# Kernel optimization log

Measured on AMD Instinct MI355X. Metric: run time of the kernel, lower is better.

## Reference

```python
import jax, jax.numpy as jnp
import numpy as np

N_FEAT = 128      # node_feat_size
HID = 128         # hidden_size
NUM_SEM = 64
N_ITER = 2
E_TYPES = 8
MAX_CHILDS = 65536
NUM_EDGES = 1048576


def setup_inputs() -> dict:
    key = jax.random.key(0)
    ks = jax.random.split(key, 12)
    d_in = N_FEAT + NUM_SEM
    inp = {
        "child_feats": jax.random.normal(ks[0], (1, MAX_CHILDS, d_in), jnp.float32),
        "child_exists": jax.random.uniform(ks[1], (1, MAX_CHILDS, 1), jnp.float32),
        "edge_type_onehot": jax.random.uniform(ks[2], (1, NUM_EDGES, E_TYPES), jnp.float32),
        "edge_indices": jax.random.randint(ks[3], (1, NUM_EDGES, 2), 0, MAX_CHILDS, jnp.int32),
        # learned params (PyTorch Linear: y = x @ W.T + b; store transposed)
        "W_child": jax.random.normal(ks[4], (d_in, HID), jnp.float32) / np.sqrt(d_in),
        "b_child": jnp.zeros((HID,), jnp.float32),
        "W_edge": jax.random.normal(ks[5], (N_ITER, 2 * HID + E_TYPES, HID), jnp.float32) / np.sqrt(2 * HID + E_TYPES),
        "b_edge": jnp.zeros((N_ITER, HID), jnp.float32),
        "W_parent": jax.random.normal(ks[6], ((N_ITER + 1) * HID, N_FEAT), jnp.float32) / np.sqrt((N_ITER + 1) * HID),
        "b_parent": jnp.zeros((N_FEAT,), jnp.float32),
    }
    return inp


def reference(child_feats, child_exists, edge_type_onehot, edge_indices,
              W_child, b_child, W_edge, b_edge, W_parent, b_parent):
    # batch_size == 1 enforced by original module
    x = jax.nn.relu(child_feats[0] @ W_child + b_child) * child_exists[0]  # (N, H)
    src = edge_indices[0, :, 0]  # (E,)
    dst = edge_indices[0, :, 1]  # (E,)
    ef = edge_type_onehot[0]     # (E, T)

    # node_symmetric_type == 'max' readout
    parent_feats = [jnp.max(x, axis=0)]
    for i in range(N_ITER):
        # gather endpoints, concat with edge features, small MLP
        nef = jnp.concatenate([x[src], x[dst], ef], axis=1)          # (E, 2H+T)
        nef = jax.nn.relu(nef @ W_edge[i] + b_edge[i])               # (E, H)
        # edge_symmetric_type == 'sum' -> scatter_add to source nodes
        x = jax.ops.segment_sum(nef, src, num_segments=MAX_CHILDS)   # (N, H)
        parent_feats.append(jnp.max(x, axis=0))

    parent_feat = jnp.concatenate(parent_feats)[None, :]             # (1, (I+1)*H)
    return jax.nn.relu(parent_feat @ W_parent + b_parent)            # (1, node_feat)
```

## Files before the change

### kernel.cpp

```cpp
#include <hip/hip_runtime.h>
#include <hip/hip_bf16.h>

#define HID 128
#define DIN 192
#define NCH 65536
#define NE  1048576

typedef __bf16 bfrag __attribute__((ext_vector_type(8)));
typedef float  ffrag __attribute__((ext_vector_type(4)));

static __device__ __forceinline__ __bf16 f2bf(float x) { return (__bf16)x; }
static __device__ __forceinline__ unsigned pk2(float a, float b) {
    __bf16 b0 = f2bf(a), b1 = f2bf(b);
    return (unsigned)*(unsigned short*)&b0 | ((unsigned)*(unsigned short*)&b1 << 16);
}
static __device__ __forceinline__ unsigned char f2q(float x) {
    return (unsigned char)(__builtin_amdgcn_cvt_pk_fp8_f32(x, x, 0, false) & 0xff);
}

struct FragsQ { long d[4]; long ef; };

__global__ __launch_bounds__(256) void k_childhist(
    const float* __restrict__ cf, const float* __restrict__ exists,
    const float* __restrict__ Wc, const float* __restrict__ bc,
    __bf16* __restrict__ xA, unsigned int* __restrict__ pmax,
    const int* __restrict__ eidx, int* __restrict__ deg)
{
    if (blockIdx.x >= 1024) {
        const int base = (blockIdx.x - 1024) * 1024 + threadIdx.x;
        #pragma unroll
        for (int k = 0; k < 4; ++k)
            atomicAdd(&deg[eidx[2 * (base + k * 256)]], 1);
        return;
    }

    __shared__ __bf16 Wl[6 * 8 * 64 * 8];
    __shared__ float  bl[HID];
    __shared__ unsigned int cm[HID];
    const int t = threadIdx.x;

    for (int idx = t; idx < DIN * HID; idx += 256) {
        int k = idx >> 7, h = idx & 127;
        int kt = k >> 5, kk = k & 31;
        int lane = ((kk >> 3) << 4) | (h & 15);
        Wl[((((kt * 8) + (h >> 4)) * 64 + lane) << 3) | (kk & 7)] = f2bf(Wc[idx]);
    }
    for (int idx = t; idx < HID; idx += 256) { bl[idx] = bc[idx]; cm[idx] = 0u; }
    __syncthreads();

    const int wave = t >> 6, lane = t & 63;
    const int m = lane & 15, quad = lane >> 4;

    const int tile = blockIdx.x * 4 + wave;
    const int r0 = tile << 4;
    const int row = r0 + m;

    ffrag acc[8];
    #pragma unroll
    for (int u = 0; u < 8; ++u)
        #pragma unroll
        for (int r = 0; r < 4; ++r) acc[u][r] = 0.f;

    const float* arow = cf + (size_t)row * DIN + quad * 8;
    #pragma unroll
    for (int kt = 0; kt < 6; ++kt) {
        float4 f0 = *(const float4*)(arow + kt * 32);
        float4 f1 = *(const float4*)(arow + kt * 32 + 4);
        bfrag a;
        a[0]=f2bf(f0.x); a[1]=f2bf(f0.y); a[2]=f2bf(f0.z); a[3]=f2bf(f0.w);
        a[4]=f2bf(f1.x); a[5]=f2bf(f1.y); a[6]=f2bf(f1.z); a[7]=f2bf(f1.w);
        #pragma unroll
        for (int u = 0; u < 8; ++u) {
            bfrag b = *(const bfrag*)(&Wl[(((kt * 8 + u) * 64 + lane) << 3)]);
            acc[u] = __builtin_amdgcn_mfma_f32_16x16x32_bf16(a, b, acc[u], 0, 0, 0);
        }
    }

    float mxu[8];
    #pragma unroll
    for (int u = 0; u < 8; ++u) mxu[u] = 0.f;

    #pragma unroll
    for (int r = 0; r < 4; ++r) {
        int er = r0 + quad * 4 + r;
        float exv = exists[er];
        __bf16* orow = xA + (size_t)er * HID;
        #pragma unroll
        for (int u = 0; u < 8; ++u) {
            int col = u * 16 + m;
            float v = fmaxf(acc[u][r] + bl[col], 0.f) * exv;
            orow[col] = f2bf(v);
            mxu[u] = fmaxf(mxu[u], v);
        }
    }
    #pragma unroll
    for (int u = 0; u < 8; ++u) {
        float v = mxu[u];
        v = fmaxf(v, __shfl_xor(v, 16));
        v = fmaxf(v, __shfl_xor(v, 32));
        if (quad == 0) atomicMax(&cm[u * 16 + m], __float_as_uint(v));
    }
    __syncthreads();
    if (t < HID) atomicMax(&pmax[t], cm[t]);
}

__global__ __launch_bounds__(256) void k_scan1(
    const int* __restrict__ deg, int* __restrict__ bsum)
{
    const int b = blockIdx.x, t = threadIdx.x;
    int v = deg[b * 256 + t];
    #pragma unroll
    for (int o = 1; o < 64; o <<= 1) v += __shfl_xor(v, o);
    __shared__ int ws[4];
    if ((t & 63) == 0) ws[t >> 6] = v;
    __syncthreads();
    if (t == 0) bsum[b] = ws[0] + ws[1] + ws[2] + ws[3];
}

__global__ __launch_bounds__(256) void k_scan2(
    const int* __restrict__ bsum, int* __restrict__ bbase)
{
    __shared__ int sc[256];
    const int t = threadIdx.x;
    int v = bsum[t];
    sc[t] = v;
    __syncthreads();
    for (int o = 1; o < 256; o <<= 1) {
        int u = (t >= o) ? sc[t - o] : 0;
        __syncthreads();
        sc[t] += u;
        __syncthreads();
    }
    bbase[t] = sc[t] - v;
}

__global__ __launch_bounds__(256) void k_scan3(
    const int* __restrict__ deg, const int* __restrict__ bbase,
    int* __restrict__ off, int* __restrict__ cursor)
{
    __shared__ int sc[256];
    const int b = blockIdx.x, t = threadIdx.x;
    int v = deg[b * 256 + t];
    sc[t] = v;
    __syncthreads();
    for (int o = 1; o < 256; o <<= 1) {
        int u = (t >= o) ? sc[t - o] : 0;
        __syncthreads();
        sc[t] += u;
        __syncthreads();
    }
    int excl = bbase[b] + sc[t] - v;
    off[b * 256 + t] = excl;
    cursor[b * 256 + t] = excl;
    if (b == 255 && t == 255) off[NCH] = excl + v;
}

__global__ __launch_bounds__(256) void k_scatter(
    const int* __restrict__ eidx, int* __restrict__ cursor,
    const float* __restrict__ ef,
    int* __restrict__ dsts, unsigned char* __restrict__ efs8)
{
    int e = blockIdx.x * 256 + threadIdx.x;
    int s = eidx[2 * e], d = eidx[2 * e + 1];
    const float4* p = (const float4*)(ef + (size_t)e * 8);
    float4 f0 = p[0], f1 = p[1];
    int pos = atomicAdd(&cursor[s], 1);
    dsts[pos] = d;
    unsigned p01 = __builtin_amdgcn_cvt_pk_fp8_f32(f0.x, f0.y, 0, false) & 0xffff;
    unsigned p23 = __builtin_amdgcn_cvt_pk_fp8_f32(f0.z, f0.w, 0, false) & 0xffff;
    unsigned p45 = __builtin_amdgcn_cvt_pk_fp8_f32(f1.x, f1.y, 0, false) & 0xffff;
    unsigned p67 = __builtin_amdgcn_cvt_pk_fp8_f32(f1.z, f1.w, 0, false) & 0xffff;
    unsigned long long v = (unsigned long long)(p01 | (p23 << 16))
                         | ((unsigned long long)(p45 | (p67 << 16)) << 32);
    *(unsigned long long*)(efs8 + (size_t)pos * 8) = v;
}

__global__ __launch_bounds__(256) void k_src(
    const __bf16* __restrict__ xCur, const float* __restrict__ We,
    const float* __restrict__ be, __bf16* __restrict__ St2,
    unsigned char* __restrict__ Dq)
{
    __shared__ __bf16 Wl[4 * 8 * 64 * 8];
    __shared__ float  bl[HID];
    const int t = threadIdx.x;
    const int wave = t >> 6, lane = t & 63;
    const int m = lane & 15, quad = lane >> 4;
    const int tile = blockIdx.x * 4 + wave;
    const int r0 = tile << 4;
    const int row = r0 + m;

    for (int idx = t; idx < 128 * HID; idx += 256) {
        int k = idx >> 7, h = idx & 127;
        int kt = k >> 5, kk = k & 31;
        int ln = ((kk >> 3) << 4) | (h & 15);
        Wl[((((kt * 8) + (h >> 4)) * 64 + ln) << 3) | (kk & 7)] = f2bf(We[idx]);
    }
    for (int idx = t; idx < HID; idx += 256) bl[idx] = be[idx];
    __syncthreads();

    bfrag a[4];
    const __bf16* ar = xCur + (size_t)row * HID + quad * 8;
    #pragma unroll
    for (int kt = 0; kt < 4; ++kt) a[kt] = *(const bfrag*)(ar + kt * 32);

    ffrag acc[8];
    #pragma unroll
    for (int u = 0; u < 8; ++u)
        #pragma unroll
        for (int r = 0; r < 4; ++r) acc[u][r] = 0.f;

    #pragma unroll
    for (int kt = 0; kt < 4; ++kt)
        #pragma unroll
        for (int u = 0; u < 8; ++u) {
            bfrag b = *(const bfrag*)(&Wl[(((kt * 8 + u) * 64 + lane) << 3)]);
            acc[u] = __builtin_amdgcn_mfma_f32_16x16x32_bf16(a[kt], b, acc[u], 0, 0, 0);
        }
    #pragma unroll
    for (int r = 0; r < 4; ++r) {
        int node = r0 + quad * 4 + r;
        bfrag pk;
        #pragma unroll
        for (int u = 0; u < 8; ++u) pk[u] = f2bf(acc[u][r] + bl[u * 16 + m]);
        *(bfrag*)(St2 + ((size_t)node * 16 + m) * 8) = pk;
    }
    __syncthreads();

    for (int idx = t; idx < 128 * HID; idx += 256) {
        int k = idx >> 7, h = idx & 127;
        int kt = k >> 5, kk = k & 31;
        int ln = ((kk >> 3) << 4) | (h & 15);
        Wl[((((kt * 8) + (h >> 4)) * 64 + ln) << 3) | (kk & 7)] = f2bf(We[(size_t)(128 + k) * HID + h]);
    }
    __syncthreads();

    #pragma unroll
    for (int u = 0; u < 8; ++u)
        #pragma unroll
        for (int r = 0; r < 4; ++r) acc[u][r] = 0.f;

    #pragma unroll
    for (int kt = 0; kt < 4; ++kt)
        #pragma unroll
        for (int u = 0; u < 8; ++u) {
            bfrag b = *(const bfrag*)(&Wl[(((kt * 8 + u) * 64 + lane) << 3)]);
            acc[u] = __builtin_amdgcn_mfma_f32_16x16x32_bf16(a[kt], b, acc[u], 0, 0, 0);
        }
    #pragma unroll
    for (int r = 0; r < 4; ++r) {
        int node = r0 + quad * 4 + r;
        unsigned char* orow = Dq + (size_t)node * 128;
        #pragma unroll
        for (int u = 0; u < 8; ++u) orow[u * 16 + m] = f2q(acc[u][r]);
    }
}

__global__ __launch_bounds__(256) void k_edge2(
    const unsigned char* __restrict__ Dq,
    const int*    __restrict__ offs,
    const int*    __restrict__ dsts,
    const unsigned char* __restrict__ efs8,
    const __bf16* __restrict__ St2,
    const float*  __restrict__ We,
    __bf16* __restrict__ xNext,
    unsigned int* __restrict__ pmax, int stage)
{
    __shared__ unsigned char Wf[8 * 16 * 8];
    __shared__ unsigned int cm[HID];
    const int t = threadIdx.x;

    if (t < HID) cm[t] = 0u;
    for (int idx = t; idx < 8 * HID; idx += 256) {
        int k2 = idx >> 7, h = idx & 127;
        Wf[((((h >> 4) * 16) + (h & 15)) << 3) + k2] = f2q(We[(size_t)(256 + k2) * HID + h]);
    }
    __syncthreads();

    const int wave = t >> 6, lane = t & 63;
    const int m = lane & 15, quad = lane >> 4;
    const int gw = blockIdx.x * 4 + wave;
    const int n0 = gw * 4;

    const long BevQ = (quad == (m >> 3))     ? ((long)0x38 << (8 * (m & 7))) : 0L;
    const long BodQ = (quad == 2 + (m >> 3)) ? ((long)0x38 << (8 * (m & 7))) : 0L;

    const int o0 = offs[n0],     o1 = offs[n0 + 1], o2 = offs[n0 + 2];
    const int o3 = offs[n0 + 3], o4 = offs[n0 + 4];

    auto selo = [&](int q) -> int {
        return (q <= 0) ? o0 : (q == 1) ? o1 : (q == 2) ? o2 : (q == 3) ? o3 : o4;
    };

    float mxu[8];
    #pragma unroll
    for (int u = 0; u < 8; ++u) mxu[u] = 0.f;

    if (o0 < o4) {
        const int dvA = dsts[min(o0 + lane, o4 - 1)];
        const int dvB = dsts[min(o0 + 64 + lane, o4 - 1)];

        auto LOADT = [&](int j) -> FragsQ {
            FragsQ f;
            int jl = j + m; jl = (jl < o4) ? jl : (o4 - 1);
            int rel = jl - o0;
            int dA = __shfl(dvA, rel & 63);
            int dB = __shfl(dvB, rel & 63);
            int dm;
            if (rel < 64)       dm = dA;
            else if (rel < 128) dm = dB;
            else                dm = dsts[jl];
            const unsigned char* rd = Dq + (size_t)dm * 128 + quad * 8;
            f.d[0] = *(const long*)(rd);
            f.d[1] = *(const long*)(rd + 32);
            f.d[2] = *(const long*)(rd + 64);
            f.d[3] = *(const long*)(rd + 96);
            f.ef = (quad == 0) ? *(const long*)(efs8 + (size_t)jl * 8) : 0L;
            return f;
        };

        int ci = 0;
        while (selo(ci) == selo(ci + 1)) ++ci;
        int cj = selo(ci);

        bfrag sb = *(const bfrag*)(St2 + ((size_t)(n0 + ci) * 16 + m) * 8);
        float part[8];
        #pragma unroll
        for (int u = 0; u < 8; ++u) part[u] = 0.f;

        FragsQ aC = LOADT(cj);

        for (;;) {
            const int cEnd = selo(ci + 1);
            int ni = ci, nj = cj + 16;
            if (nj >= cEnd) {
                ni = ci + 1;
                while (ni < 4 && selo(ni) == selo(ni + 1)) ++ni;
                nj = (ni < 4) ? selo(ni) : 0;
            }
            const bool hn = (ni < 4);
            FragsQ aN;
            if (hn) aN = LOADT(nj);

            ffrag acc[8];
            #pragma unroll
            for (int u = 0; u < 8; ++u) {
                float s = (float)sb[u];
                acc[u][0] = s; acc[u][1] = s; acc[u][2] = s; acc[u][3] = s;
            }
            #pragma unroll
            for (int u = 0; u < 8; ++u)
                acc[u] = __builtin_amdgcn_mfma_f32_16x16x32_fp8_fp8(
                    aC.d[u >> 1], (u & 1) ? BodQ : BevQ, acc[u], 0, 0, 0);
            #pragma unroll
            for (int u = 0; u < 8; ++u) {
                long b = *(const long*)(&Wf[((u << 4) + m) << 3]);
                acc[u] = __builtin_amdgcn_mfma_f32_16x16x32_fp8_fp8(aC.ef, b, acc[u], 0, 0, 0);
            }

            const int rb = cj + quad * 4;
            #pragma unroll
            for (int r = 0; r < 4; ++r) {
                if (rb + r < cEnd) {
                    #pragma unroll
                    for (int u = 0; u < 8; ++u)
                        part[u] += fmaxf(acc[u][r], 0.f);
                }
            }

            if (!hn || ni != ci) {
                float tot[8];
                #pragma unroll
                for (int u = 0; u < 8; ++u) {
                    float v = part[u];
                    v += __shfl_xor(v, 16);
                    v += __shfl_xor(v, 32);
                    tot[u] = v;
                    mxu[u] = fmaxf(mxu[u], v);
                }
                float sA = (quad == 0) ? tot[0] : (quad == 1) ? tot[2] : (quad == 2) ? tot[4] : tot[6];
                float sB = (quad == 0) ? tot[1] : (quad == 1) ? tot[3] : (quad == 2) ? tot[5] : tot[7];
                const int n = n0 + ci, u0 = quad * 2;
                xNext[(size_t)n * HID + u0 * 16 + m]      = f2bf(sA);
                xNext[(size_t)n * HID + u0 * 16 + 16 + m] = f2bf(sB);
                if (hn) {
                    sb = *(const bfrag*)(St2 + ((size_t)(n0 + ni) * 16 + m) * 8);
                    #pragma unroll
                    for (int u = 0; u < 8; ++u) part[u] = 0.f;
                }
            }
            if (!hn) break;
            aC = aN; ci = ni; cj = nj;
        }
    }

    {
        const int u0 = quad * 2;
        const __bf16 zz = (__bf16)0.f;
        if (o0 == o1) { xNext[(size_t)(n0+0)*HID + u0*16 + m] = zz; xNext[(size_t)(n0+0)*HID + u0*16 + 16 + m] = zz; }
        if (o1 == o2) { xNext[(size_t)(n0+1)*HID + u0*16 + m] = zz; xNext[(size_t)(n0+1)*HID + u0*16 + 16 + m] = zz; }
        if (o2 == o3) { xNext[(size_t)(n0+2)*HID + u0*16 + m] = zz; xNext[(size_t)(n0+2)*HID + u0*16 + 16 + m] = zz; }
        if (o3 == o4) { xNext[(size_t)(n0+3)*HID + u0*16 + m] = zz; xNext[(size_t)(n0+3)*HID + u0*16 + 16 + m] = zz; }
    }

    #pragma unroll
    for (int u = 0; u < 8; ++u) {
        float v = mxu[u];
        v = fmaxf(v, __shfl_xor(v, 16));
        v = fmaxf(v, __shfl_xor(v, 32));
        if (quad == 0) atomicMax(&cm[u * 16 + m], __float_as_uint(v));
    }
    __syncthreads();
    if (t < HID) atomicMax(&pmax[stage * HID + t], cm[t]);
}

__global__ __launch_bounds__(256) void k_edge_at(
    const __bf16* __restrict__ xA, const int* __restrict__ eidx,
    const float* __restrict__ ef, const float* __restrict__ We,
    const float* __restrict__ be, float* __restrict__ xNew)
{
    __shared__ __bf16 Wl[9 * 8 * 64 * 8];
    __shared__ float  bl[HID];
    const int t = threadIdx.x;
    for (int idx = t; idx < 8 * 64 * 8; idx += 256) Wl[8 * 8 * 64 * 8 + idx] = (__bf16)0.f;
    __syncthreads();
    for (int idx = t; idx < 256 * HID; idx += 256) {
        int k = idx >> 7, h = idx & 127;
        int kt = k >> 5, kk = k & 31;
        int lane = ((kk >> 3) << 4) | (h & 15);
        Wl[((((kt * 8) + (h >> 4)) * 64 + lane) << 3) | (kk & 7)] = f2bf(We[idx]);
    }
    for (int idx = t; idx < 8 * HID; idx += 256) {
        int k2 = idx >> 7, h = idx & 127;
        Wl[((((8 * 8) + (h >> 4)) * 64 + (h & 15)) << 3) | k2] = f2bf(We[(256 + k2) * HID + h]);
    }
    for (int idx = t; idx < HID; idx += 256) bl[idx] = be[idx];
    __syncthreads();

    const int wave = t >> 6, lane = t & 63;
    const int m = lane & 15, quad = lane >> 4;
    for (int c = 0; c < 8; ++c) {
        const int e0 = blockIdx.x * 512 + c * 64 + wave * 16;
        const int e  = e0 + m;
        const int src = eidx[2 * e], dst = eidx[2 * e + 1];
        const __bf16* rs = xA + (size_t)src * HID;
        const __bf16* rd = xA + (size_t)dst * HID;
        bfrag a[9];
        #pragma unroll
        for (int kt = 0; kt < 4; ++kt) a[kt] = *(const bfrag*)(rs + kt * 32 + quad * 8);
        #pragma unroll
        for (int kt = 4; kt < 8; ++kt) a[kt] = *(const bfrag*)(rd + (kt - 4) * 32 + quad * 8);
        {
            bfrag z;
            #pragma unroll
            for (int q = 0; q < 8; ++q) z[q] = (__bf16)0.f;
            if (quad == 0) {
                const float4* p = (const float4*)(ef + (size_t)e * 8);
                float4 f0 = p[0], f1 = p[1];
                z[0]=f2bf(f0.x); z[1]=f2bf(f0.y); z[2]=f2bf(f0.z); z[3]=f2bf(f0.w);
                z[4]=f2bf(f1.x); z[5]=f2bf(f1.y); z[6]=f2bf(f1.z); z[7]=f2bf(f1.w);
            }
            a[8] = z;
        }
        ffrag acc[8];
        #pragma unroll
        for (int u = 0; u < 8; ++u)
            #pragma unroll
            for (int r = 0; r < 4; ++r) acc[u][r] = 0.f;
        #pragma unroll
        for (int kt = 0; kt < 9; ++kt)
            #pragma unroll
            for (int u = 0; u < 8; ++u) {
                bfrag b = *(const bfrag*)(&Wl[(((kt * 8 + u) * 64 + lane) << 3)]);
                acc[u] = __builtin_amdgcn_mfma_f32_16x16x32_bf16(a[kt], b, acc[u], 0, 0, 0);
            }
        #pragma unroll
        for (int r = 0; r < 4; ++r) {
            int er = e0 + quad * 4 + r;
            int sr = eidx[2 * er];
            float* outrow = xNew + (size_t)sr * HID;
            #pragma unroll
            for (int u = 0; u < 8; ++u) {
                int col = u * 16 + m;
                atomicAdd(outrow + col, fmaxf(acc[u][r] + bl[col], 0.f));
            }
        }
    }
}

__global__ __launch_bounds__(256) void k_fin(
    float* __restrict__ xNew, __bf16* __restrict__ xA,
    unsigned int* __restrict__ pmax, int stage, int flags)
{
    const int t = threadIdx.x;
    const size_t total  = (size_t)NCH * HID;
    const size_t stride = (size_t)gridDim.x * 256;
    float mx = 0.f;
    for (size_t i = (size_t)blockIdx.x * 256 + t; i < total; i += stride) {
        float v = xNew[i];
        mx = fmaxf(mx, v);
        if (flags & 1) xA[i] = f2bf(v);
        if (flags & 2) xNew[i] = 0.f;
    }
    __shared__ float red[256];
    red[t] = mx;
    __syncthreads();
    if (t < 128) {
        float v = fmaxf(red[t], red[t + 128]);
        atomicMax(&pmax[stage * HID + t], __float_as_uint(v));
    }
}

__global__ __launch_bounds__(128) void k_parent(
    const unsigned int* __restrict__ pmaxU,
    const float* __restrict__ Wp, const float* __restrict__ bp,
    float* __restrict__ out)
{
    __shared__ float pl[384];
    const int t = threadIdx.x;
    for (int i = t; i < 384; i += 128) pl[i] = __uint_as_float(pmaxU[i]);
    __syncthreads();
    float acc = bp[t];
    for (int j = 0; j < 384; ++j) acc += pl[j] * Wp[j * HID + t];
    out[t] = fmaxf(acc, 0.f);
}

extern "C" void kernel_launch(void* const* d_in, const int* in_sizes, int n_in,
                              void* d_out, int out_size, void* d_ws, size_t ws_size,
                              hipStream_t stream)
{
    const float* cf   = (const float*)d_in[0];
    const float* ex   = (const float*)d_in[1];
    const float* ef   = (const float*)d_in[2];
    const int*   eidx = (const int*)d_in[3];
    const float* Wc   = (const float*)d_in[4];
    const float* bc   = (const float*)d_in[5];
    const float* We   = (const float*)d_in[6];
    const float* be   = (const float*)d_in[7];
    const float* Wp   = (const float*)d_in[8];
    const float* bp   = (const float*)d_in[9];
    float* out = (float*)d_out;

    char* ws = (char*)d_ws;

    const size_t OFF_XA   = 0;
    const size_t OFF_XB   = OFF_XA   + (size_t)NCH * HID * 2;
    const size_t OFF_ST   = OFF_XB   + (size_t)NCH * HID * 2;
    const size_t OFF_EFS  = OFF_ST   + (size_t)NCH * HID * 2;
    const size_t OFF_DQ   = OFF_EFS  + (size_t)NE * 8;
    const size_t OFF_DST  = OFF_DQ   + (size_t)NCH * 128;
    const size_t OFF_OFFS = OFF_DST  + (size_t)NE * 4;
    const size_t OFF_DEG  = OFF_OFFS + 262400;
    const size_t OFF_CUR  = OFF_DEG  + 262144;
    const size_t OFF_PMAX = OFF_CUR  + 262144;
    const size_t OFF_BS   = OFF_PMAX + 2048;
    const size_t OFF_BB   = OFF_BS   + 1024;
    const size_t NEED     = OFF_BB   + 1024;

    if (ws_size >= NEED) {
        __bf16*        xA   = (__bf16*)(ws + OFF_XA);
        __bf16*        xB   = (__bf16*)(ws + OFF_XB);
        __bf16*        St2  = (__bf16*)(ws + OFF_ST);
        unsigned char* efs8 = (unsigned char*)(ws + OFF_EFS);
        unsigned char* Dq   = (unsigned char*)(ws + OFF_DQ);
        int*           dsts = (int*)   (ws + OFF_DST);
        int*           offs = (int*)   (ws + OFF_OFFS);
        int*           deg  = (int*)   (ws + OFF_DEG);
        int*           cur  = (int*)   (ws + OFF_CUR);
        unsigned int*  pmax = (unsigned int*)(ws + OFF_PMAX);
        int*           bsum = (int*)   (ws + OFF_BS);
        int*           bbas = (int*)   (ws + OFF_BB);

        hipMemsetAsync(pmax, 0, 384 * sizeof(unsigned int), stream);
        hipMemsetAsync(deg, 0, NCH * sizeof(int), stream);

        k_childhist<<<2048, 256, 0, stream>>>(cf, ex, Wc, bc, xA, pmax, eidx, deg);
        k_scan1  <<<256,  256, 0, stream>>>(deg, bsum);
        k_scan2  <<<1,    256, 0, stream>>>(bsum, bbas);
        k_scan3  <<<256,  256, 0, stream>>>(deg, bbas, offs, cur);
        k_scatter<<<4096, 256, 0, stream>>>(eidx, cur, ef, dsts, efs8);

        k_src    <<<1024, 256, 0, stream>>>(xA, We, be, St2, Dq);
        k_edge2  <<<4096, 256, 0, stream>>>(Dq, offs, dsts, efs8, St2, We, xB, pmax, 1);
        k_src    <<<1024, 256, 0, stream>>>(xB, We + 264 * HID, be + HID, St2, Dq);
        k_edge2  <<<4096, 256, 0, stream>>>(Dq, offs, dsts, efs8, St2, We + 264 * HID, xA, pmax, 2);
        k_parent <<<1,    128, 0, stream>>>(pmax, Wp, bp, out);
    } else {
        float*        xNew = (float*)ws;
        __bf16*       xA   = (__bf16*)(ws + (size_t)NCH * HID * 4);
        unsigned int* pmax = (unsigned int*)(ws + (size_t)NCH * HID * 6);

        hipMemsetAsync(pmax, 0, 384 * sizeof(unsigned int), stream);
        hipMemsetAsync(xNew, 0, (size_t)NCH * HID * 4, stream);

        k_childhist<<<1024, 256, 0, stream>>>(cf, ex, Wc, bc, xA, pmax, eidx, (int*)nullptr);
        k_edge_at<<<2048, 256, 0, stream>>>(xA, eidx, ef, We,             be,       xNew);
        k_fin    <<<512,  256, 0, stream>>>(xNew, xA, pmax, 1, 3);
        k_edge_at<<<2048, 256, 0, stream>>>(xA, eidx, ef, We + 264 * HID, be + HID, xNew);
        k_fin    <<<512,  256, 0, stream>>>(xNew, xA, pmax, 2, 0);
        k_parent <<<1,    128, 0, stream>>>(pmax, Wp, bp, out);
    }
}
```

Before: 538.6 us.

## Fuse scan and scatter kernels, restage weights, repack Dq for wider loads

Merges the scan2 and scan3 passes into one kernel in which every block redundantly scans the block sums. The edge scatter is folded into the first source-projection launch as extra blocks. The two memsets become one by placing pmax next to deg. Weight staging now writes whole 8-element bf16 fragments per thread, and the Dq fp8 layout is permuted so each lane reads two 16-byte vectors instead of four 8-byte loads. The aim is fewer launches, less launch and serialization overhead, and wider memory accesses, at the cost of redundant scan work in each block.

```diff
diff --git a/kernel.cpp b/kernel.cpp
--- a/kernel.cpp
+++ b/kernel.cpp
@@ -8,6 +8,7 @@
 
 typedef __bf16 bfrag __attribute__((ext_vector_type(8)));
 typedef float  ffrag __attribute__((ext_vector_type(4)));
+typedef long   lfrag2 __attribute__((ext_vector_type(2)));
 
 static __device__ __forceinline__ __bf16 f2bf(float x) { return (__bf16)x; }
 static __device__ __forceinline__ unsigned pk2(float a, float b) {
@@ -19,6 +20,20 @@
 }
 
 struct FragsQ { long d[4]; long ef; };
+
+static __device__ __forceinline__ void stage_wfrag(
+    __bf16* Wl, const float* W, int rowoff, int chunks, int t)
+{
+    for (int c = t; c < chunks; c += 256) {
+        int lane = c & 63, u = (c >> 6) & 7, kt = c >> 9;
+        int k0 = kt * 32 + ((lane >> 4) << 3), h = u * 16 + (lane & 15);
+        const float* src = W + (size_t)(rowoff + k0) * 128 + h;
+        bfrag f;
+        #pragma unroll
+        for (int j = 0; j < 8; ++j) f[j] = f2bf(src[(size_t)j * 128]);
+        *(bfrag*)(&Wl[(size_t)c << 3]) = f;
+    }
+}
 
 __global__ __launch_bounds__(256) void k_childhist(
     const float* __restrict__ cf, const float* __restrict__ exists,
@@ -39,12 +54,7 @@
     __shared__ unsigned int cm[HID];
     const int t = threadIdx.x;
 
-    for (int idx = t; idx < DIN * HID; idx += 256) {
-        int k = idx >> 7, h = idx & 127;
-        int kt = k >> 5, kk = k & 31;
-        int lane = ((kk >> 3) << 4) | (h & 15);
-        Wl[((((kt * 8) + (h >> 4)) * 64 + lane) << 3) | (kk & 7)] = f2bf(Wc[idx]);
-    }
+    stage_wfrag(Wl, Wc, 0, 3072, t);
     for (int idx = t; idx < HID; idx += 256) { bl[idx] = bc[idx]; cm[idx] = 0u; }
     __syncthreads();
 
@@ -117,84 +127,66 @@
     if (t == 0) bsum[b] = ws[0] + ws[1] + ws[2] + ws[3];
 }
 
-__global__ __launch_bounds__(256) void k_scan2(
-    const int* __restrict__ bsum, int* __restrict__ bbase)
-{
-    __shared__ int sc[256];
-    const int t = threadIdx.x;
-    int v = bsum[t];
-    sc[t] = v;
+__global__ __launch_bounds__(256) void k_scan23(
+    const int* __restrict__ deg, const int* __restrict__ bsum,
+    int* __restrict__ off, int* __restrict__ cursor)
+{
+    __shared__ int sb[256], sc[256];
+    const int b = blockIdx.x, t = threadIdx.x;
+    int w = bsum[t];
+    int v = deg[b * 256 + t];
+    sb[t] = w; sc[t] = v;
     __syncthreads();
     for (int o = 1; o < 256; o <<= 1) {
-        int u = (t >= o) ? sc[t - o] : 0;
+        int u1 = (t >= o) ? sb[t - o] : 0;
+        int u2 = (t >= o) ? sc[t - o] : 0;
         __syncthreads();
-        sc[t] += u;
+        sb[t] += u1; sc[t] += u2;
         __syncthreads();
     }
-    bbase[t] = sc[t] - v;
-}
-
-__global__ __launch_bounds__(256) void k_scan3(
-    const int* __restrict__ deg, const int* __restrict__ bbase,
-    int* __restrict__ off, int* __restrict__ cursor)
-{
-    __shared__ int sc[256];
-    const int b = blockIdx.x, t = threadIdx.x;
-    int v = deg[b * 256 + t];
-    sc[t] = v;
-    __syncthreads();
-    for (int o = 1; o < 256; o <<= 1) {
-        int u = (t >= o) ? sc[t - o] : 0;
-        __syncthreads();
-        sc[t] += u;
-        __syncthreads();
-    }
-    int excl = bbase[b] + sc[t] - v;
+    int bbase = (b == 0) ? 0 : sb[b - 1];
+    int excl = bbase + sc[t] - v;
     off[b * 256 + t] = excl;
     cursor[b * 256 + t] = excl;
     if (b == 255 && t == 255) off[NCH] = excl + v;
 }
 
-__global__ __launch_bounds__(256) void k_scatter(
+__global__ __launch_bounds__(256) void k_scsrc(
+    const __bf16* __restrict__ xCur, const float* __restrict__ We,
+    const float* __restrict__ be, __bf16* __restrict__ St2,
+    unsigned char* __restrict__ Dq,
     const int* __restrict__ eidx, int* __restrict__ cursor,
     const float* __restrict__ ef,
     int* __restrict__ dsts, unsigned char* __restrict__ efs8)
 {
-    int e = blockIdx.x * 256 + threadIdx.x;
-    int s = eidx[2 * e], d = eidx[2 * e + 1];
-    const float4* p = (const float4*)(ef + (size_t)e * 8);
-    float4 f0 = p[0], f1 = p[1];
-    int pos = atomicAdd(&cursor[s], 1);
-    dsts[pos] = d;
-    unsigned p01 = __builtin_amdgcn_cvt_pk_fp8_f32(f0.x, f0.y, 0, false) & 0xffff;
-    unsigned p23 = __builtin_amdgcn_cvt_pk_fp8_f32(f0.z, f0.w, 0, false) & 0xffff;
-    unsigned p45 = __builtin_amdgcn_cvt_pk_fp8_f32(f1.x, f1.y, 0, false) & 0xffff;
-    unsigned p67 = __builtin_amdgcn_cvt_pk_fp8_f32(f1.z, f1.w, 0, false) & 0xffff;
-    unsigned long long v = (unsigned long long)(p01 | (p23 << 16))
-                         | ((unsigned long long)(p45 | (p67 << 16)) << 32);
-    *(unsigned long long*)(efs8 + (size_t)pos * 8) = v;
-}
-
-__global__ __launch_bounds__(256) void k_src(
-    const __bf16* __restrict__ xCur, const float* __restrict__ We,
-    const float* __restrict__ be, __bf16* __restrict__ St2,
-    unsigned char* __restrict__ Dq)
-{
     __shared__ __bf16 Wl[4 * 8 * 64 * 8];
     __shared__ float  bl[HID];
     const int t = threadIdx.x;
+
+    if (blockIdx.x >= 1024) {
+        int e = (blockIdx.x - 1024) * 256 + t;
+        int s = eidx[2 * e], d = eidx[2 * e + 1];
+        const float4* p = (const float4*)(ef + (size_t)e * 8);
+        float4 f0 = p[0], f1 = p[1];
+        int pos = atomicAdd(&cursor[s], 1);
+        dsts[pos] = d;
+        unsigned p01 = __builtin_amdgcn_cvt_pk_fp8_f32(f0.x, f0.y, 0, false) & 0xffff;
+        unsigned p23 = __builtin_amdgcn_cvt_pk_fp8_f32(f0.z, f0.w, 0, false) & 0xffff;
+        unsigned p45 = __builtin_amdgcn_cvt_pk_fp8_f32(f1.x, f1.y, 0, false) & 0xffff;
+        unsigned p67 = __builtin_amdgcn_cvt_pk_fp8_f32(f1.z, f1.w, 0, false) & 0xffff;
+        unsigned long long v = (unsigned long long)(p01 | (p23 << 16))
+                             | ((unsigned long long)(p45 | (p67 << 16)) << 32);
+        *(unsigned long long*)(efs8 + (size_t)pos * 8) = v;
+        return;
+    }
+
     const int wave = t >> 6, lane = t & 63;
     const int m = lane & 15, quad = lane >> 4;
     const int tile = blockIdx.x * 4 + wave;
     const int r0 = tile << 4;
     const int row = r0 + m;
 
-    for (int idx = t; idx < 128 * HID; idx += 256) {
-        int k = idx >> 7, h = idx & 127;
-        int kt = k >> 5, kk = k & 31;
-        int ln = ((kk >> 3) << 4) | (h & 15);
-        Wl[((((kt * 8) + (h >> 4)) * 64 + ln) << 3) | (kk & 7)] = f2bf(We[idx]);
-    }
+    stage_wfrag(Wl, We, 0, 2048, t);
     for (int idx = t; idx < HID; idx += 256) bl[idx] = be[idx];
     __syncthreads();
 
@@ -226,12 +218,7 @@
     }
     __syncthreads();
 
-    for (int idx = t; idx < 128 * HID; idx += 256) {
-        int k = idx >> 7, h = idx & 127;
-        int kt = k >> 5, kk = k & 31;
-        int ln = ((kk >> 3) << 4) | (h & 15);
-        Wl[((((kt * 8) + (h >> 4)) * 64 + ln) << 3) | (kk & 7)] = f2bf(We[(size_t)(128 + k) * HID + h]);
-    }
+    stage_wfrag(Wl, We, 128, 2048, t);
     __syncthreads();
 
     #pragma unroll
@@ -251,7 +238,8 @@
         int node = r0 + quad * 4 + r;
         unsigned char* orow = Dq + (size_t)node * 128;
         #pragma unroll
-        for (int u = 0; u < 8; ++u) orow[u * 16 + m] = f2q(acc[u][r]);
+        for (int u = 0; u < 8; ++u)
+            orow[((u & 1) * 2 + (m >> 3)) * 32 + (u >> 1) * 8 + (m & 7)] = f2q(acc[u][r]);
     }
 }
 
@@ -309,11 +297,10 @@
             if (rel < 64)       dm = dA;
             else if (rel < 128) dm = dB;
             else                dm = dsts[jl];
-            const unsigned char* rd = Dq + (size_t)dm * 128 + quad * 8;
-            f.d[0] = *(const long*)(rd);
-            f.d[1] = *(const long*)(rd + 32);
-            f.d[2] = *(const long*)(rd + 64);
-            f.d[3] = *(const long*)(rd + 96);
+            const unsigned char* rd = Dq + (size_t)dm * 128 + quad * 32;
+            lfrag2 w0 = *(const lfrag2*)(rd);
+            lfrag2 w1 = *(const lfrag2*)(rd + 16);
+            f.d[0] = w0[0]; f.d[1] = w0[1]; f.d[2] = w1[0]; f.d[3] = w1[1];
             f.ef = (quad == 0) ? *(const long*)(efs8 + (size_t)jl * 8) : 0L;
             return f;
         };
@@ -423,12 +410,7 @@
     const int t = threadIdx.x;
     for (int idx = t; idx < 8 * 64 * 8; idx += 256) Wl[8 * 8 * 64 * 8 + idx] = (__bf16)0.f;
     __syncthreads();
-    for (int idx = t; idx < 256 * HID; idx += 256) {
-        int k = idx >> 7, h = idx & 127;
-        int kt = k >> 5, kk = k & 31;
-        int lane = ((kk >> 3) << 4) | (h & 15);
-        Wl[((((kt * 8) + (h >> 4)) * 64 + lane) << 3) | (kk & 7)] = f2bf(We[idx]);
-    }
+    stage_wfrag(Wl, We, 0, 4096, t);
     for (int idx = t; idx < 8 * HID; idx += 256) {
         int k2 = idx >> 7, h = idx & 127;
         Wl[((((8 * 8) + (h >> 4)) * 64 + (h & 15)) << 3) | k2] = f2bf(We[(256 + k2) * HID + h]);
@@ -550,11 +532,10 @@
     const size_t OFF_DST  = OFF_DQ   + (size_t)NCH * 128;
     const size_t OFF_OFFS = OFF_DST  + (size_t)NE * 4;
     const size_t OFF_DEG  = OFF_OFFS + 262400;
-    const size_t OFF_CUR  = OFF_DEG  + 262144;
-    const size_t OFF_PMAX = OFF_CUR  + 262144;
-    const size_t OFF_BS   = OFF_PMAX + 2048;
-    const size_t OFF_BB   = OFF_BS   + 1024;
-    const size_t NEED     = OFF_BB   + 1024;
+    const size_t OFF_PMAX = OFF_DEG  + 262144;
+    const size_t OFF_CUR  = OFF_PMAX + 2048;
+    const size_t OFF_BS   = OFF_CUR  + 262144;
+    const size_t NEED     = OFF_BS   + 1024;
 
     if (ws_size >= NEED) {
         __bf16*        xA   = (__bf16*)(ws + OFF_XA);
@@ -568,20 +549,18 @@
         int*           cur  = (int*)   (ws + OFF_CUR);
         unsigned int*  pmax = (unsigned int*)(ws + OFF_PMAX);
         int*           bsum = (int*)   (ws + OFF_BS);
-        int*           bbas = (int*)   (ws + OFF_BB);
-
-        hipMemsetAsync(pmax, 0, 384 * sizeof(unsigned int), stream);
-        hipMemsetAsync(deg, 0, NCH * sizeof(int), stream);
+
+        hipMemsetAsync(deg, 0, 262144 + 2048, stream);
 
         k_childhist<<<2048, 256, 0, stream>>>(cf, ex, Wc, bc, xA, pmax, eidx, deg);
         k_scan1  <<<256,  256, 0, stream>>>(deg, bsum);
-        k_scan2  <<<1,    256, 0, stream>>>(bsum, bbas);
-        k_scan3  <<<256,  256, 0, stream>>>(deg, bbas, offs, cur);
-        k_scatter<<<4096, 256, 0, stream>>>(eidx, cur, ef, dsts, efs8);
-
-        k_src    <<<1024, 256, 0, stream>>>(xA, We, be, St2, Dq);
+        k_scan23 <<<256,  256, 0, stream>>>(deg, bsum, offs, cur);
+
+        k_scsrc  <<<5120, 256, 0, stream>>>(xA, We, be, St2, Dq,
+                                            eidx, cur, ef, dsts, efs8);
         k_edge2  <<<4096, 256, 0, stream>>>(Dq, offs, dsts, efs8, St2, We, xB, pmax, 1);
-        k_src    <<<1024, 256, 0, stream>>>(xB, We + 264 * HID, be + HID, St2, Dq);
+        k_scsrc  <<<1024, 256, 0, stream>>>(xB, We + 264 * HID, be + HID, St2, Dq,
+                                            eidx, cur, ef, dsts, efs8);
         k_edge2  <<<4096, 256, 0, stream>>>(Dq, offs, dsts, efs8, St2, We + 264 * HID, xA, pmax, 2);
         k_parent <<<1,    128, 0, stream>>>(pmax, Wp, bp, out);
     } else {
```

After: 518.8 us. 1.04x faster.
